# Kernel tuning notes

Measured on AMD Instinct MI355X. Metric: run time of the kernel, lower is better.

## Reference

```python
import jax, jax.numpy as jnp
import numpy as np


def setup_inputs() -> dict:
    key = jax.random.key(0)
    k1, k2 = jax.random.split(key)
    decoder_state_t = jax.random.normal(k1, (32, 256), dtype=jnp.float32)
    encoder_states = jax.random.normal(k2, (32, 8192, 256), dtype=jnp.float32)
    return {"decoder_state_t": decoder_state_t, "encoder_states": encoder_states}


def reference(decoder_state_t, encoder_states):
    # score[b, s] = sum_h decoder_state_t[b, h] * encoder_states[b, s, h]
    score = jnp.einsum("bh,bsh->bs", decoder_state_t, encoder_states)
    atten_prob = jax.nn.softmax(score, axis=-1)            # (bs, source_length)
    # context[b, h] = sum_s atten_prob[b, s] * encoder_states[b, s, h]
    context = jnp.einsum("bs,bsh->bh", atten_prob, encoder_states)
    return (atten_prob, context)
```

## Files before the change

### kernel.cpp

```cpp
#include <hip/hip_runtime.h>
#include <math.h>

#define B_ 32
#define S_ 8192
#define H_ 256
#define CHUNK_ 512
#define WAVES_PB 4
#define WROWS (CHUNK_ / WAVES_PB)
#define TILE_ 16
#define NCHUNK (S_ / CHUNK_)
#define NPART (B_ * NCHUNK * WAVES_PB)
#define PPB (NCHUNK * WAVES_PB)

__global__ __launch_bounds__(256) void
k1_flash(const float* __restrict__ dec, const float* __restrict__ enc,
         float* __restrict__ scores_out, float* __restrict__ pm,
         float* __restrict__ pl, float* __restrict__ pc) {
    const int lane  = threadIdx.x & 63;
    const int wave  = threadIdx.x >> 6;
    const int batch = blockIdx.x >> 4;
    const int chunk = blockIdx.x & (NCHUNK - 1);
    const int rowBase = chunk * CHUNK_ + wave * WROWS;

    const float4 d = *(const float4*)(dec + batch * H_ + lane * 4);
    const float* ebase = enc + (size_t)batch * S_ * H_;

    float  m = -INFINITY, l = 0.f;
    float4 c = make_float4(0.f, 0.f, 0.f, 0.f);

    for (int t = 0; t < WROWS / TILE_; ++t) {
        const int r0 = rowBase + t * TILE_;
        float4 v[TILE_];
        float  sc[TILE_];
#pragma unroll
        for (int r = 0; r < TILE_; ++r) {
            v[r] = *(const float4*)(ebase + (size_t)(r0 + r) * H_ + lane * 4);
            float sp = v[r].x * d.x + v[r].y * d.y + v[r].z * d.z + v[r].w * d.w;
#pragma unroll
            for (int off = 32; off; off >>= 1) sp += __shfl_xor(sp, off);
            sc[r] = sp;
        }
        float tmax = sc[0];
#pragma unroll
        for (int r = 1; r < TILE_; ++r) tmax = fmaxf(tmax, sc[r]);
        const float mnew = fmaxf(m, tmax);
        const float f = __expf(m - mnew);
        c.x *= f; c.y *= f; c.z *= f; c.w *= f;
        l *= f;
        m = mnew;
#pragma unroll
        for (int r = 0; r < TILE_; ++r) {
            const float p = __expf(sc[r] - m);
            l += p;
            c.x += p * v[r].x;
            c.y += p * v[r].y;
            c.z += p * v[r].z;
            c.w += p * v[r].w;
        }
        if (lane == 0) {
            float* so = scores_out + batch * S_ + r0;
            *(float4*)(so + 0)  = make_float4(sc[0],  sc[1],  sc[2],  sc[3]);
            *(float4*)(so + 4)  = make_float4(sc[4],  sc[5],  sc[6],  sc[7]);
            *(float4*)(so + 8)  = make_float4(sc[8],  sc[9],  sc[10], sc[11]);
            *(float4*)(so + 12) = make_float4(sc[12], sc[13], sc[14], sc[15]);
        }
    }

    const int pid = blockIdx.x * WAVES_PB + wave;
    *(float4*)(pc + (size_t)pid * H_ + lane * 4) = c;
    if (lane == 0) { pm[pid] = m; pl[pid] = l; }
}

__global__ __launch_bounds__(256) void
k2_combine(const float* __restrict__ pm, const float* __restrict__ pl,
           const float* __restrict__ pc, float* __restrict__ ctx_out,
           float* __restrict__ fm, float* __restrict__ frl) {
    const int b = blockIdx.x;
    const int h = threadIdx.x;
    float M = -INFINITY;
    for (int i = 0; i < PPB; ++i) M = fmaxf(M, pm[b * PPB + i]);
    float L = 0.f, acc = 0.f;
    for (int i = 0; i < PPB; ++i) {
        const float w = __expf(pm[b * PPB + i] - M);
        L   += w * pl[b * PPB + i];
        acc += w * pc[(size_t)(b * PPB + i) * H_ + h];
    }
    ctx_out[b * H_ + h] = acc / L;
    if (h == 0) { fm[b] = M; frl[b] = 1.f / L; }
}

__global__ __launch_bounds__(256) void
k3_prob(float* __restrict__ probs, const float* __restrict__ fm,
        const float* __restrict__ frl) {
    const int i = blockIdx.x * blockDim.x + threadIdx.x;
    const int b = i / (S_ / 4);
    float4 v = ((const float4*)probs)[i];
    const float M = fm[b], R = frl[b];
    v.x = __expf(v.x - M) * R;
    v.y = __expf(v.y - M) * R;
    v.z = __expf(v.z - M) * R;
    v.w = __expf(v.w - M) * R;
    ((float4*)probs)[i] = v;
}

extern "C" void kernel_launch(void* const* d_in, const int* in_sizes, int n_in,
                              void* d_out, int out_size, void* d_ws, size_t ws_size,
                              hipStream_t stream) {
    const float* dec = (const float*)d_in[0];
    const float* enc = (const float*)d_in[1];
    float* out    = (float*)d_out;
    float* scores = out;
    float* ctx    = out + B_ * S_;

    float* pm  = (float*)d_ws;
    float* pl  = pm + NPART;
    float* pc  = pl + NPART;
    float* fm  = pc + (size_t)NPART * H_;
    float* frl = fm + B_;

    k1_flash<<<B_ * NCHUNK, 256, 0, stream>>>(dec, enc, scores, pm, pl, pc);
    k2_combine<<<B_, 256, 0, stream>>>(pm, pl, pc, ctx, fm, frl);
    k3_prob<<<(B_ * S_ / 4) / 256, 256, 0, stream>>>(scores, fm, frl);
}
```

Measured before the change: 57.90 us.

## Fuse combine and probability normalization into one kernel with wave-level reductions

The separate combine and normalization kernels are merged into one launch. Each block recomputes the per-batch max and normalizer from the 64 partials using wave shuffles, so the normalization blocks no longer have to wait for a combine kernel. Context blocks use shuffle-broadcast weights instead of serial scalar loops over the partials. This removes one kernel launch and the serial dependency between the two steps, at the cost of recomputing the reductions redundantly in every block.

```diff
diff --git a/kernel.cpp b/kernel.cpp
--- a/kernel.cpp
+++ b/kernel.cpp
@@ -72,35 +72,51 @@
 }
 
 __global__ __launch_bounds__(256) void
-k2_combine(const float* __restrict__ pm, const float* __restrict__ pl,
-           const float* __restrict__ pc, float* __restrict__ ctx_out,
-           float* __restrict__ fm, float* __restrict__ frl) {
-    const int b = blockIdx.x;
-    const int h = threadIdx.x;
-    float M = -INFINITY;
-    for (int i = 0; i < PPB; ++i) M = fmaxf(M, pm[b * PPB + i]);
-    float L = 0.f, acc = 0.f;
-    for (int i = 0; i < PPB; ++i) {
-        const float w = __expf(pm[b * PPB + i] - M);
-        L   += w * pl[b * PPB + i];
-        acc += w * pc[(size_t)(b * PPB + i) * H_ + h];
+k23_finish(const float* __restrict__ pm, const float* __restrict__ pl,
+           const float* __restrict__ pc, float* __restrict__ probs,
+           float* __restrict__ ctx_out) {
+    const int lane = threadIdx.x & 63;
+
+    if (blockIdx.x < 256) {
+        const int b = blockIdx.x >> 3;
+        const float pmv = pm[b * PPB + lane];
+        const float plv = pl[b * PPB + lane];
+        float M = pmv;
+#pragma unroll
+        for (int off = 32; off; off >>= 1) M = fmaxf(M, __shfl_xor(M, off));
+        float Lp = __expf(pmv - M) * plv;
+#pragma unroll
+        for (int off = 32; off; off >>= 1) Lp += __shfl_xor(Lp, off);
+        const float R = 1.f / Lp;
+
+        float* p = probs + b * S_ + (blockIdx.x & 7) * 1024 + threadIdx.x * 4;
+        float4 v = *(const float4*)p;
+        v.x = __expf(v.x - M) * R;
+        v.y = __expf(v.y - M) * R;
+        v.z = __expf(v.z - M) * R;
+        v.w = __expf(v.w - M) * R;
+        *(float4*)p = v;
+    } else {
+        const int b = blockIdx.x - 256;
+        const int h = threadIdx.x;
+        const float pmv = pm[b * PPB + lane];
+        const float plv = pl[b * PPB + lane];
+        float M = pmv;
+#pragma unroll
+        for (int off = 32; off; off >>= 1) M = fmaxf(M, __shfl_xor(M, off));
+        const float w = __expf(pmv - M);
+        float L = w * plv;
+#pragma unroll
+        for (int off = 32; off; off >>= 1) L += __shfl_xor(L, off);
+
+        float acc = 0.f;
+        const float* pcb = pc + (size_t)b * PPB * H_ + h;
+#pragma unroll 8
+        for (int i = 0; i < PPB; ++i) {
+            acc += __shfl(w, i) * pcb[(size_t)i * H_];
+        }
+        ctx_out[b * H_ + h] = acc / L;
     }
-    ctx_out[b * H_ + h] = acc / L;
-    if (h == 0) { fm[b] = M; frl[b] = 1.f / L; }
-}
-
-__global__ __launch_bounds__(256) void
-k3_prob(float* __restrict__ probs, const float* __restrict__ fm,
-        const float* __restrict__ frl) {
-    const int i = blockIdx.x * blockDim.x + threadIdx.x;
-    const int b = i / (S_ / 4);
-    float4 v = ((const float4*)probs)[i];
-    const float M = fm[b], R = frl[b];
-    v.x = __expf(v.x - M) * R;
-    v.y = __expf(v.y - M) * R;
-    v.z = __expf(v.z - M) * R;
-    v.w = __expf(v.w - M) * R;
-    ((float4*)probs)[i] = v;
 }
 
 extern "C" void kernel_launch(void* const* d_in, const int* in_sizes, int n_in,
@@ -112,13 +128,10 @@
     float* scores = out;
     float* ctx    = out + B_ * S_;
 
-    float* pm  = (float*)d_ws;
-    float* pl  = pm + NPART;
-    float* pc  = pl + NPART;
-    float* fm  = pc + (size_t)NPART * H_;
-    float* frl = fm + B_;
+    float* pm = (float*)d_ws;
+    float* pl = pm + NPART;
+    float* pc = pl + NPART;
 
     k1_flash<<<B_ * NCHUNK, 256, 0, stream>>>(dec, enc, scores, pm, pl, pc);
-    k2_combine<<<B_, 256, 0, stream>>>(pm, pl, pc, ctx, fm, frl);
-    k3_prob<<<(B_ * S_ / 4) / 256, 256, 0, stream>>>(scores, fm, frl);
+    k23_finish<<<256 + B_, 256, 0, stream>>>(pm, pl, pc, scores, ctx);
 }
```

Result: faster. 52.15 us (-9.9%).
